# Performance work log

Measured on AMD Instinct MI355X. Metric: run time of the kernel, lower is better.

Reference implementation:

```python
import jax, jax.numpy as jnp
import numpy as np

BINS = 30
PAD_IDX = 0


def setup_inputs() -> dict:
    key = jax.random.key(0)
    k1, k2, k3 = jax.random.split(key, 3)
    B, Q, D = 128, 32, 8192
    # cosine similarity matrix in [-1, 1]
    simmat = jax.random.uniform(k1, (B, Q, D), jnp.float32, minval=-1.0, maxval=1.0)
    dtoks = jax.random.randint(k2, (B, D), 0, 32000)
    qtoks = jax.random.randint(k3, (B, Q), 0, 32000)
    return {"simmat": simmat, "dtoks": dtoks, "qtoks": qtoks}


def reference(simmat, dtoks, qtoks):
    B, Q, D = simmat.shape
    # map similarity in [-1,1] to integer bin in [0, BINS-1] (truncating cast, same as torch .int())
    bins = ((simmat + 1.000001) / 2.0 * (BINS - 1)).astype(jnp.int32)  # [B,Q,D]
    # weight = 1 where neither the doc token nor the query token is padding
    w = ((dtoks[:, None, :] != PAD_IDX) & (qtoks[:, :, None] != PAD_IDX)).astype(simmat.dtype)  # [B,Q,D]
    # fused weighted bincount for all (b,q) rows in one scatter-add:
    # global segment id = row_index * BINS + bin
    row_offsets = jnp.arange(B * Q, dtype=jnp.int32)[:, None] * BINS  # [B*Q,1]
    seg_ids = (bins.reshape(B * Q, D) + row_offsets).reshape(-1)
    hist = jax.ops.segment_sum(w.reshape(-1), seg_ids, num_segments=B * Q * BINS)
    hist = hist.reshape(B, Q, BINS)
    return jnp.log(hist + 1e-5)
```

## Files before the change

### kernel.cpp

```cpp
#include <hip/hip_runtime.h>
#include <math.h>

#define BINS 30
#define QDIM 32
#define DDIM 8192

__global__ __launch_bounds__(256) void drmm_hist_kernel(
    const float* __restrict__ simmat,
    const int*   __restrict__ dtoks,
    const int*   __restrict__ qtoks,
    float*       __restrict__ out)
{
    const int bq = blockIdx.x;
    const int b  = bq >> 5;
    const int t  = threadIdx.x;
    const int wv = t >> 6;

    __shared__ int hist[4][32];
    if (t < 128) ((int*)hist)[t] = 0;
    __syncthreads();

    const bool qvalid = (qtoks[bq] != 0);

    const float4* __restrict__ srow = reinterpret_cast<const float4*>(simmat + (size_t)bq * DDIM);
    const int4*   __restrict__ drow = reinterpret_cast<const int4*>(dtoks + (size_t)b * DDIM);

    int* __restrict__ h = hist[wv];

#pragma unroll
    for (int it = 0; it < 8; ++it) {
        const int v = it * 256 + t;
        const float4 s  = srow[v];
        const int4   dt = drow[v];

        int bin0 = (int)(((s.x + 1.000001f) / 2.0f) * 29.0f);
        int bin1 = (int)(((s.y + 1.000001f) / 2.0f) * 29.0f);
        int bin2 = (int)(((s.z + 1.000001f) / 2.0f) * 29.0f);
        int bin3 = (int)(((s.w + 1.000001f) / 2.0f) * 29.0f);
        bin0 = min(max(bin0, 0), BINS - 1);
        bin1 = min(max(bin1, 0), BINS - 1);
        bin2 = min(max(bin2, 0), BINS - 1);
        bin3 = min(max(bin3, 0), BINS - 1);

        if (qvalid) {
            if (dt.x != 0) atomicAdd(&h[bin0], 1);
            if (dt.y != 0) atomicAdd(&h[bin1], 1);
            if (dt.z != 0) atomicAdd(&h[bin2], 1);
            if (dt.w != 0) atomicAdd(&h[bin3], 1);
        }
    }
    __syncthreads();

    if (t < BINS) {
        const int c = hist[0][t] + hist[1][t] + hist[2][t] + hist[3][t];
        out[(size_t)bq * BINS + t] = logf((float)c + 1e-5f);
    }
}

extern "C" void kernel_launch(void* const* d_in, const int* in_sizes, int n_in,
                              void* d_out, int out_size, void* d_ws, size_t ws_size,
                              hipStream_t stream) {
    const float* simmat = (const float*)d_in[0];
    const int*   dtoks  = (const int*)d_in[1];
    const int*   qtoks  = (const int*)d_in[2];
    float*       out    = (float*)d_out;

    const int BQ = in_sizes[2];
    drmm_hist_kernel<<<BQ, 256, 0, stream>>>(simmat, dtoks, qtoks, out);
}
```

Baseline: 32.68 us.

## Precompute doc padding bitmask in a prepass and stage it in LDS

Adds a prepass kernel that packs the dtoks nonzero test into a bitmask with wave ballots. The histogram kernel then loads each batch row's 1 KB mask into shared memory instead of re-reading 32 KB of dtoks for every (b,q) block, and it skips the simmat loads entirely when the query token is padding. The goal is to cut redundant global traffic for dtoks, at the cost of an extra kernel launch and a dependency on the workspace buffer.

After: 32.56 us. About the same (-0.4%).

```diff
diff --git a/kernel.cpp b/kernel.cpp
--- a/kernel.cpp
+++ b/kernel.cpp
@@ -4,10 +4,23 @@
 #define BINS 30
 #define QDIM 32
 #define DDIM 8192
+#define MASK_WORDS_PER_ROW 256
+
+__global__ __launch_bounds__(256) void build_mask_kernel(
+    const int* __restrict__ dtoks,
+    unsigned int* __restrict__ mask)
+{
+    const int gid = blockIdx.x * 256 + threadIdx.x;
+    const int tok = dtoks[gid];
+    const unsigned long long bal = __ballot(tok != 0);
+    if ((threadIdx.x & 63) == 0) {
+        reinterpret_cast<unsigned long long*>(mask)[gid >> 6] = bal;
+    }
+}
 
 __global__ __launch_bounds__(256) void drmm_hist_kernel(
     const float* __restrict__ simmat,
-    const int*   __restrict__ dtoks,
+    const unsigned int* __restrict__ mask,
     const int*   __restrict__ qtoks,
     float*       __restrict__ out)
 {
@@ -17,36 +30,39 @@
     const int wv = t >> 6;
 
     __shared__ int hist[4][32];
+    __shared__ unsigned int mask_lds[MASK_WORDS_PER_ROW];
+
     if (t < 128) ((int*)hist)[t] = 0;
+    mask_lds[t] = mask[b * MASK_WORDS_PER_ROW + t];
     __syncthreads();
 
     const bool qvalid = (qtoks[bq] != 0);
 
-    const float4* __restrict__ srow = reinterpret_cast<const float4*>(simmat + (size_t)bq * DDIM);
-    const int4*   __restrict__ drow = reinterpret_cast<const int4*>(dtoks + (size_t)b * DDIM);
-
-    int* __restrict__ h = hist[wv];
+    if (qvalid) {
+        const float4* __restrict__ srow =
+            reinterpret_cast<const float4*>(simmat + (size_t)bq * DDIM);
+        int* __restrict__ h = hist[wv];
 
 #pragma unroll
-    for (int it = 0; it < 8; ++it) {
-        const int v = it * 256 + t;
-        const float4 s  = srow[v];
-        const int4   dt = drow[v];
+        for (int it = 0; it < 8; ++it) {
+            const int v = it * 256 + t;
+            const float4 s = srow[v];
+            const unsigned int bits =
+                (mask_lds[it * 32 + (t >> 3)] >> ((t & 7) * 4)) & 0xFu;
 
-        int bin0 = (int)(((s.x + 1.000001f) / 2.0f) * 29.0f);
-        int bin1 = (int)(((s.y + 1.000001f) / 2.0f) * 29.0f);
-        int bin2 = (int)(((s.z + 1.000001f) / 2.0f) * 29.0f);
-        int bin3 = (int)(((s.w + 1.000001f) / 2.0f) * 29.0f);
-        bin0 = min(max(bin0, 0), BINS - 1);
-        bin1 = min(max(bin1, 0), BINS - 1);
-        bin2 = min(max(bin2, 0), BINS - 1);
-        bin3 = min(max(bin3, 0), BINS - 1);
+            int bin0 = (int)(((s.x + 1.000001f) / 2.0f) * 29.0f);
+            int bin1 = (int)(((s.y + 1.000001f) / 2.0f) * 29.0f);
+            int bin2 = (int)(((s.z + 1.000001f) / 2.0f) * 29.0f);
+            int bin3 = (int)(((s.w + 1.000001f) / 2.0f) * 29.0f);
+            bin0 = min(max(bin0, 0), BINS - 1);
+            bin1 = min(max(bin1, 0), BINS - 1);
+            bin2 = min(max(bin2, 0), BINS - 1);
+            bin3 = min(max(bin3, 0), BINS - 1);
 
-        if (qvalid) {
-            if (dt.x != 0) atomicAdd(&h[bin0], 1);
-            if (dt.y != 0) atomicAdd(&h[bin1], 1);
-            if (dt.z != 0) atomicAdd(&h[bin2], 1);
-            if (dt.w != 0) atomicAdd(&h[bin3], 1);
+            if (bits & 1u) atomicAdd(&h[bin0], 1);
+            if (bits & 2u) atomicAdd(&h[bin1], 1);
+            if (bits & 4u) atomicAdd(&h[bin2], 1);
+            if (bits & 8u) atomicAdd(&h[bin3], 1);
         }
     }
     __syncthreads();
@@ -66,5 +82,11 @@
     float*       out    = (float*)d_out;
 
     const int BQ = in_sizes[2];
-    drmm_hist_kernel<<<BQ, 256, 0, stream>>>(simmat, dtoks, qtoks, out);
+    const int B  = BQ / QDIM;
+    const int ntok = B * DDIM;
+
+    unsigned int* mask = (unsigned int*)d_ws;
+
+    build_mask_kernel<<<ntok / 256, 256, 0, stream>>>(dtoks, mask);
+    drmm_hist_kernel<<<BQ, 256, 0, stream>>>(simmat, mask, qtoks, out);
 }
```

## Spread histogram over 8 lane-interleaved copies and loop blocks over two rows

Applied to the files above, without the earlier changes.

Replaces the per-wave shared histogram with 8 interleaved copies indexed by lane, so atomics from neighbouring lanes land on different addresses and banks and contend less. Masked elements go to an extra dump bin instead of a divergent branch. The grid is fixed at 2048 blocks, each handling two (b,q) rows, and launch bounds request 8 blocks per CU. The risks are that the row count is hardcoded to 4096, and masked elements now always issue atomics.

New measurement: 31.40 us. 3.9% less time.

```diff
diff --git a/kernel.cpp b/kernel.cpp
--- a/kernel.cpp
+++ b/kernel.cpp
@@ -4,56 +4,64 @@
 #define BINS 30
 #define QDIM 32
 #define DDIM 8192
+#define NCOPY 8
+#define NBLK 2048
 
-__global__ __launch_bounds__(256) void drmm_hist_kernel(
+__global__ __launch_bounds__(256, 8) void drmm_hist_kernel(
     const float* __restrict__ simmat,
     const int*   __restrict__ dtoks,
     const int*   __restrict__ qtoks,
     float*       __restrict__ out)
 {
-    const int bq = blockIdx.x;
-    const int b  = bq >> 5;
-    const int t  = threadIdx.x;
-    const int wv = t >> 6;
+    const int t = threadIdx.x;
+    const int c = t & (NCOPY - 1);
 
-    __shared__ int hist[4][32];
-    if (t < 128) ((int*)hist)[t] = 0;
-    __syncthreads();
+    __shared__ int hist[(BINS + 1) * NCOPY];
 
-    const bool qvalid = (qtoks[bq] != 0);
+    for (int bq = blockIdx.x; bq < NBLK * 2; bq += NBLK) {
+        const int b = bq >> 5;
 
-    const float4* __restrict__ srow = reinterpret_cast<const float4*>(simmat + (size_t)bq * DDIM);
-    const int4*   __restrict__ drow = reinterpret_cast<const int4*>(dtoks + (size_t)b * DDIM);
+        if (t < (BINS + 1) * NCOPY) hist[t] = 0;
+        __syncthreads();
 
-    int* __restrict__ h = hist[wv];
+        const bool qvalid = (qtoks[bq] != 0);
+        const float4* __restrict__ srow =
+            reinterpret_cast<const float4*>(simmat + (size_t)bq * DDIM);
+        const int4* __restrict__ drow =
+            reinterpret_cast<const int4*>(dtoks + (size_t)b * DDIM);
 
 #pragma unroll
-    for (int it = 0; it < 8; ++it) {
-        const int v = it * 256 + t;
-        const float4 s  = srow[v];
-        const int4   dt = drow[v];
+        for (int it = 0; it < 8; ++it) {
+            const int v = it * 256 + t;
+            const float4 s  = srow[v];
+            const int4   dt = drow[v];
 
-        int bin0 = (int)(((s.x + 1.000001f) / 2.0f) * 29.0f);
-        int bin1 = (int)(((s.y + 1.000001f) / 2.0f) * 29.0f);
-        int bin2 = (int)(((s.z + 1.000001f) / 2.0f) * 29.0f);
-        int bin3 = (int)(((s.w + 1.000001f) / 2.0f) * 29.0f);
-        bin0 = min(max(bin0, 0), BINS - 1);
-        bin1 = min(max(bin1, 0), BINS - 1);
-        bin2 = min(max(bin2, 0), BINS - 1);
-        bin3 = min(max(bin3, 0), BINS - 1);
+            int bin0 = (int)(((s.x + 1.000001f) / 2.0f) * 29.0f);
+            int bin1 = (int)(((s.y + 1.000001f) / 2.0f) * 29.0f);
+            int bin2 = (int)(((s.z + 1.000001f) / 2.0f) * 29.0f);
+            int bin3 = (int)(((s.w + 1.000001f) / 2.0f) * 29.0f);
+            bin0 = min(max(bin0, 0), BINS - 1);
+            bin1 = min(max(bin1, 0), BINS - 1);
+            bin2 = min(max(bin2, 0), BINS - 1);
+            bin3 = min(max(bin3, 0), BINS - 1);
+            bin0 = (qvalid && dt.x != 0) ? bin0 : BINS;
+            bin1 = (qvalid && dt.y != 0) ? bin1 : BINS;
+            bin2 = (qvalid && dt.z != 0) ? bin2 : BINS;
+            bin3 = (qvalid && dt.w != 0) ? bin3 : BINS;
 
-        if (qvalid) {
-            if (dt.x != 0) atomicAdd(&h[bin0], 1);
-            if (dt.y != 0) atomicAdd(&h[bin1], 1);
-            if (dt.z != 0) atomicAdd(&h[bin2], 1);
-            if (dt.w != 0) atomicAdd(&h[bin3], 1);
+            atomicAdd(&hist[bin0 * NCOPY + c], 1);
+            atomicAdd(&hist[bin1 * NCOPY + c], 1);
+            atomicAdd(&hist[bin2 * NCOPY + c], 1);
+            atomicAdd(&hist[bin3 * NCOPY + c], 1);
         }
-    }
-    __syncthreads();
+        __syncthreads();
 
-    if (t < BINS) {
-        const int c = hist[0][t] + hist[1][t] + hist[2][t] + hist[3][t];
-        out[(size_t)bq * BINS + t] = logf((float)c + 1e-5f);
+        if (t < BINS) {
+            const int* h = &hist[t * NCOPY];
+            const int cnt = h[0] + h[1] + h[2] + h[3] + h[4] + h[5] + h[6] + h[7];
+            out[(size_t)bq * BINS + t] = logf((float)cnt + 1e-5f);
+        }
+        __syncthreads();
     }
 }
 
@@ -65,6 +73,5 @@
     const int*   qtoks  = (const int*)d_in[2];
     float*       out    = (float*)d_out;
 
-    const int BQ = in_sizes[2];
-    drmm_hist_kernel<<<BQ, 256, 0, stream>>>(simmat, dtoks, qtoks, out);
+    drmm_hist_kernel<<<NBLK, 256, 0, stream>>>(simmat, dtoks, qtoks, out);
 }
```

## Precompute doc-padding bitmask and spread histogram over 32 LDS copies

Applied to the files above, without the earlier changes.

Adds a pre-pass kernel that packs the doc-token nonzero flags into one 32-bit mask per thread, so the histogram kernel reads 4 bytes per thread instead of re-reading int4 dtoks for every query row. The histogram is replicated 32 times in shared memory, indexed by lane, to cut atomic contention, and is reduced with shuffles at the end. Padded query rows now exit early. The bin clamp is dropped and the scale is folded into a single multiply. The cost is a second kernel launch, a workspace buffer, and atomics that add 0 for padded tokens.

Measured after the change: 31.05 us. 1.05x faster.

```diff
diff --git a/kernel.cpp b/kernel.cpp
--- a/kernel.cpp
+++ b/kernel.cpp
@@ -4,56 +4,77 @@
 #define BINS 30
 #define QDIM 32
 #define DDIM 8192
+#define NCOPY 32
 
-__global__ __launch_bounds__(256) void drmm_hist_kernel(
+__global__ __launch_bounds__(256) void build_mask_kernel(
+    const int* __restrict__ dtoks,
+    unsigned int* __restrict__ pmask)
+{
+    const int b = blockIdx.x;
+    const int t = threadIdx.x;
+    const int4* __restrict__ drow = reinterpret_cast<const int4*>(dtoks + (size_t)b * DDIM);
+    unsigned int bits = 0u;
+#pragma unroll
+    for (int it = 0; it < 8; ++it) {
+        const int4 dt = drow[it * 256 + t];
+        bits |= (dt.x != 0 ? 1u : 0u) << (4 * it + 0);
+        bits |= (dt.y != 0 ? 1u : 0u) << (4 * it + 1);
+        bits |= (dt.z != 0 ? 1u : 0u) << (4 * it + 2);
+        bits |= (dt.w != 0 ? 1u : 0u) << (4 * it + 3);
+    }
+    pmask[b * 256 + t] = bits;
+}
+
+__global__ __launch_bounds__(256, 8) void drmm_hist_kernel(
     const float* __restrict__ simmat,
-    const int*   __restrict__ dtoks,
+    const unsigned int* __restrict__ pmask,
     const int*   __restrict__ qtoks,
     float*       __restrict__ out)
 {
     const int bq = blockIdx.x;
     const int b  = bq >> 5;
     const int t  = threadIdx.x;
-    const int wv = t >> 6;
+    const int c  = t & (NCOPY - 1);
 
-    __shared__ int hist[4][32];
-    if (t < 128) ((int*)hist)[t] = 0;
+    __shared__ int hist[32 * NCOPY];
+
+    reinterpret_cast<int4*>(hist)[t] = int4{0, 0, 0, 0};
+
+    if (qtoks[bq] == 0) {
+        if (t < BINS) out[(size_t)bq * BINS + t] = logf(1e-5f);
+        return;
+    }
+
+    const unsigned int nib = pmask[b * 256 + t];
+    const float4* __restrict__ srow =
+        reinterpret_cast<const float4*>(simmat + (size_t)bq * DDIM);
+
     __syncthreads();
-
-    const bool qvalid = (qtoks[bq] != 0);
-
-    const float4* __restrict__ srow = reinterpret_cast<const float4*>(simmat + (size_t)bq * DDIM);
-    const int4*   __restrict__ drow = reinterpret_cast<const int4*>(dtoks + (size_t)b * DDIM);
-
-    int* __restrict__ h = hist[wv];
 
 #pragma unroll
     for (int it = 0; it < 8; ++it) {
-        const int v = it * 256 + t;
-        const float4 s  = srow[v];
-        const int4   dt = drow[v];
+        const float4 s = srow[it * 256 + t];
+        const int bin0 = (int)((s.x + 1.000001f) * 14.5f);
+        const int bin1 = (int)((s.y + 1.000001f) * 14.5f);
+        const int bin2 = (int)((s.z + 1.000001f) * 14.5f);
+        const int bin3 = (int)((s.w + 1.000001f) * 14.5f);
 
-        int bin0 = (int)(((s.x + 1.000001f) / 2.0f) * 29.0f);
-        int bin1 = (int)(((s.y + 1.000001f) / 2.0f) * 29.0f);
-        int bin2 = (int)(((s.z + 1.000001f) / 2.0f) * 29.0f);
-        int bin3 = (int)(((s.w + 1.000001f) / 2.0f) * 29.0f);
-        bin0 = min(max(bin0, 0), BINS - 1);
-        bin1 = min(max(bin1, 0), BINS - 1);
-        bin2 = min(max(bin2, 0), BINS - 1);
-        bin3 = min(max(bin3, 0), BINS - 1);
-
-        if (qvalid) {
-            if (dt.x != 0) atomicAdd(&h[bin0], 1);
-            if (dt.y != 0) atomicAdd(&h[bin1], 1);
-            if (dt.z != 0) atomicAdd(&h[bin2], 1);
-            if (dt.w != 0) atomicAdd(&h[bin3], 1);
-        }
+        atomicAdd(&hist[bin0 * NCOPY + c], (int)((nib >> (4 * it + 0)) & 1u));
+        atomicAdd(&hist[bin1 * NCOPY + c], (int)((nib >> (4 * it + 1)) & 1u));
+        atomicAdd(&hist[bin2 * NCOPY + c], (int)((nib >> (4 * it + 2)) & 1u));
+        atomicAdd(&hist[bin3 * NCOPY + c], (int)((nib >> (4 * it + 3)) & 1u));
     }
     __syncthreads();
 
-    if (t < BINS) {
-        const int c = hist[0][t] + hist[1][t] + hist[2][t] + hist[3][t];
-        out[(size_t)bq * BINS + t] = logf((float)c + 1e-5f);
+    if (t < BINS * 8) {
+        const int bin = t >> 3;
+        const int j   = t & 7;
+        int p = hist[bin * NCOPY + j]      + hist[bin * NCOPY + j + 8]
+              + hist[bin * NCOPY + j + 16] + hist[bin * NCOPY + j + 24];
+        p += __shfl_xor(p, 1);
+        p += __shfl_xor(p, 2);
+        p += __shfl_xor(p, 4);
+        if (j == 0) out[(size_t)bq * BINS + bin] = logf((float)p + 1e-5f);
     }
 }
 
@@ -66,5 +87,10 @@
     float*       out    = (float*)d_out;
 
     const int BQ = in_sizes[2];
-    drmm_hist_kernel<<<BQ, 256, 0, stream>>>(simmat, dtoks, qtoks, out);
+    const int B  = BQ / QDIM;
+
+    unsigned int* pmask = (unsigned int*)d_ws;
+
+    build_mask_kernel<<<B, 256, 0, stream>>>(dtoks, pmask);
+    drmm_hist_kernel<<<BQ, 256, 0, stream>>>(simmat, pmask, qtoks, out);
 }
```
